# Optimization experiments

Hardware: AMD Instinct MI355X
Metric: run time of the kernel (lower is better)

## Reference

```python
import jax, jax.numpy as jnp
import numpy as np

N = 10000      # nodes
IN_DIM = 512   # input feature dim
HID = 512      # GCN hidden dim
OUT = 256      # embedding dim
E = 320000     # edges (avg degree 32)


def _normalize(x, eps=1e-12):
    # F.normalize: x / max(||x||_2, eps), row-wise
    n = jnp.sqrt(jnp.sum(x * x, axis=-1, keepdims=True))
    return x / jnp.maximum(n, eps)


def _gcn_conv(x, W, b, src, dst, n):
    # DGL GraphConv with norm='both': D_out^{-1/2} -> sum-aggregate -> D_in^{-1/2}, then bias
    ones = jnp.ones(src.shape[0], x.dtype)
    deg_out = jax.ops.segment_sum(ones, src, num_segments=n)
    deg_in = jax.ops.segment_sum(ones, dst, num_segments=n)
    ns = jnp.where(deg_out > 0, deg_out ** -0.5, 0.0)
    nd = jnp.where(deg_in > 0, deg_in ** -0.5, 0.0)
    h = x @ W                                  # weight first (math-equivalent)
    msg = h[src] * ns[src, None]               # gather + src-normalize
    agg = jax.ops.segment_sum(msg, dst, num_segments=n)  # scatter-sum to dst
    return agg * nd[:, None] + b


def _gcn(x, params, src, dst, n):
    W0, b0, W1, b1 = params
    h = jax.nn.relu(_gcn_conv(x, W0, b0, src, dst, n))
    return _gcn_conv(h, W1, b1, src, dst, n)


def _scores(v, u, Wp, bp, src, dst, n, tau):
    # pos_score: edge sim = <normalize(u)[src], normalize(proj(v))[dst]> / tau, scatter-mean to dst
    q = _normalize(v @ Wp + bp)
    un = _normalize(u)
    sim = jnp.sum(un[src] * q[dst], axis=1) / tau          # [E]
    cnt = jax.ops.segment_sum(jnp.ones_like(sim), dst, num_segments=n)
    denom = jnp.maximum(cnt, 1.0)                          # DGL mean gives 0 for deg-0 nodes
    pos = jax.ops.segment_sum(sim, dst, num_segments=n) / denom
    # neg_score: per-node total similarity (intra + inter), then per-edge log, scatter-mean
    z = _normalize(v)
    stu = _normalize(u)
    neg_sim = jnp.exp(z @ z.T / tau).sum(1) + jnp.exp(z @ stu.T / tau).sum(1)  # [N]
    m = jnp.log(neg_sim[dst] + jnp.exp(sim))               # udf_u_add_log_e
    neg = jax.ops.segment_sum(m, dst, num_segments=n) / denom
    return pos, neg


def setup_inputs() -> dict:
    key = jax.random.key(0)
    ks = jax.random.split(key, 16)
    feat = jax.random.normal(ks[0], (N, IN_DIM), jnp.float32)
    src_g = jax.random.randint(ks[1], (E,), 0, N)
    dst_g = jax.random.randint(ks[2], (E,), 0, N)
    src_s = jax.random.randint(ks[3], (E,), 0, N)
    dst_s = jax.random.randint(ks[4], (E,), 0, N)

    def lin(k, i, o, s=0.05):
        return jax.random.normal(k, (i, o), jnp.float32) * s

    inp = dict(
        feat=feat, src_g=src_g, dst_g=dst_g, src_s=src_s, dst_s=dst_s,
        tau1=jnp.ones((), jnp.float32), tau2=jnp.ones((), jnp.float32),
        # encoder1 (GCN, 2 layers) online + target (deepcopy -> independent params)
        W1a=lin(ks[5], IN_DIM, HID), b1a=jnp.zeros((HID,), jnp.float32),
        W1b=lin(ks[6], HID, OUT), b1b=jnp.zeros((OUT,), jnp.float32),
        W1a_t=lin(ks[7], IN_DIM, HID), b1a_t=jnp.zeros((HID,), jnp.float32),
        W1b_t=lin(ks[8], HID, OUT), b1b_t=jnp.zeros((OUT,), jnp.float32),
        # encoder2 (Linear) online + target
        W2=lin(ks[9], IN_DIM, OUT), b2=jnp.zeros((OUT,), jnp.float32),
        W2_t=lin(ks[10], IN_DIM, OUT), b2_t=jnp.zeros((OUT,), jnp.float32),
        # projector: Predictor(out, out, num_layers=1) -> single Linear
        Wp=lin(ks[11], OUT, OUT), bp=jnp.zeros((OUT,), jnp.float32),
    )
    return inp


def reference(feat, src_g, dst_g, src_s, dst_s, tau1, tau2,
              W1a, b1a, W1b, b1b, W1a_t, b1a_t, W1b_t, b1b_t,
              W2, b2, W2_t, b2_t, Wp, bp):
    n = feat.shape[0]
    # branch 1: GCN encoder
    v1 = _gcn(feat, (W1a, b1a, W1b, b1b), src_g, dst_g, n)
    u1 = _gcn(feat, (W1a_t, b1a_t, W1b_t, b1b_t), src_g, dst_g, n)
    pos1, neg1 = _scores(v1, u1, Wp, bp, src_s, dst_s, n, tau1)
    loss1 = jnp.mean(-pos1 + neg1)
    # branch 2: linear encoder
    v2 = feat @ W2 + b2
    u2 = feat @ W2_t + b2_t
    pos2, neg2 = _scores(v2, u2, Wp, bp, src_s, dst_s, n, tau2)
    loss2 = jnp.mean(-pos2 + neg2)
    return (v1, u1, v2, u2, loss1 + loss2)
```

## Files before the change

### kernel.cpp

```cpp
#include <hip/hip_runtime.h>

typedef __bf16 bf16x8 __attribute__((ext_vector_type(8)));
typedef float f32x4 __attribute__((ext_vector_type(4)));
typedef unsigned short u16x8 __attribute__((ext_vector_type(8)));

#define GLOAD16(gp, lp) __builtin_amdgcn_global_load_lds( \
    (const __attribute__((address_space(1))) void*)(gp), \
    (__attribute__((address_space(3))) void*)(lp), 16, 0, 0)

__device__ __forceinline__ unsigned short f2bf(float f) {
  union { float f; unsigned u; } c; c.f = f;
  unsigned u = c.u;
  u = (u + 0x7fffu + ((u >> 16) & 1u)) >> 16;
  return (unsigned short)u;
}
__device__ __forceinline__ float b2f(unsigned short u) {
  union { unsigned u; float f; } c; c.u = ((unsigned)u) << 16; return c.f;
}

__global__ void k_count(const int* __restrict__ src_g, const int* __restrict__ dst_g,
                        const int* __restrict__ dst_s,
                        int* deg_og, int* deg_ig, int* cnt_s, int E)
{
  int e = blockIdx.x * blockDim.x + threadIdx.x;
  if (e >= E) return;
  atomicAdd(&deg_og[src_g[e]], 1);
  atomicAdd(&deg_ig[dst_g[e]], 1);
  atomicAdd(&cnt_s[dst_s[e]], 1);
}

__global__ void k_norms(const int* __restrict__ deg_og, const int* __restrict__ deg_ig,
                        float* __restrict__ ns, float* __restrict__ nd, int N)
{
  int i = blockIdx.x * blockDim.x + threadIdx.x;
  if (i >= N) return;
  int a = deg_og[i]; ns[i] = a > 0 ? rsqrtf((float)a) : 0.f;
  int b = deg_ig[i]; nd[i] = b > 0 ? rsqrtf((float)b) : 0.f;
}

__global__ __launch_bounds__(1024) void k_scan(const int* __restrict__ deg, int* __restrict__ offs, int N)
{
  __shared__ int lds[1024];
  __shared__ int carry_s;
  const int t = threadIdx.x;
  if (t == 0) { carry_s = 0; offs[0] = 0; }
  __syncthreads();
  for (int base = 0; base < N; base += 1024) {
    const int i = base + t;
    int v = (i < N) ? deg[i] : 0;
    lds[t] = v;
    __syncthreads();
    for (int o = 1; o < 1024; o <<= 1) {
      int tmp = (t >= o) ? lds[t - o] : 0;
      __syncthreads();
      lds[t] += tmp;
      __syncthreads();
    }
    const int carry = carry_s;
    if (i < N) offs[i + 1] = lds[t] + carry;
    __syncthreads();
    if (t == 1023) carry_s = carry + lds[1023];
    __syncthreads();
  }
}

__global__ void k_fill(const int* __restrict__ src_g, const int* __restrict__ dst_g,
                       const int* __restrict__ offs, int* cursor, int* __restrict__ csr_src, int E)
{
  int e = blockIdx.x * blockDim.x + threadIdx.x;
  if (e >= E) return;
  int d = dst_g[e];
  int p = atomicAdd(&cursor[d], 1);
  csr_src[offs[d] + p] = src_g[e];
}

struct PrepArgs {
  const float *feat, *W1a, *W1at, *W1b, *W1bt, *W2, *W2t, *Wp;
  const float *b1a, *b1at, *b1b, *b1bt, *b2, *b2t;
  unsigned short *featb, *wcatL1, *wcat2, *wcatLin, *wtp;
  float *bcatL1, *bcatGcn, *bcatLin;
  int NF;
};
__global__ void k_prep(PrepArgs p)
{
  int i = blockIdx.x * blockDim.x + threadIdx.x;
  if (i < p.NF) { p.featb[i] = f2bf(p.feat[i]); return; }
  i -= p.NF;
  if (i < 1024 * 512) {
    int n = i >> 9, k = i & 511;
    p.wcatL1[i] = f2bf(n < 512 ? p.W1a[k * 512 + n] : p.W1at[k * 512 + n - 512]);
    return;
  }
  i -= 1024 * 512;
  if (i < 512 * 512) {
    int n = i >> 9, k = i & 511;
    p.wcat2[i] = f2bf(n < 256 ? p.W1b[k * 256 + n] : p.W1bt[k * 256 + n - 256]);
    return;
  }
  i -= 512 * 512;
  if (i < 512 * 512) {
    int n = i >> 9, k = i & 511;
    p.wcatLin[i] = f2bf(n < 256 ? p.W2[k * 256 + n] : p.W2t[k * 256 + n - 256]);
    return;
  }
  i -= 512 * 512;
  if (i < 256 * 256) {
    int n = i >> 8, k = i & 255;
    p.wtp[i] = f2bf(p.Wp[k * 256 + n]);
    return;
  }
  i -= 256 * 256;
  if (i < 1024) { p.bcatL1[i] = i < 512 ? p.b1a[i] : p.b1at[i - 512]; return; }
  i -= 1024;
  if (i < 512) { p.bcatGcn[i] = i < 256 ? p.b1b[i] : p.b1bt[i - 256]; return; }
  i -= 512;
  if (i < 512) { p.bcatLin[i] = i < 256 ? p.b2[i] : p.b2t[i - 256]; return; }
}

__global__ __launch_bounds__(256) void k_mgemm(
    const unsigned short* __restrict__ A, int lda,
    const unsigned short* __restrict__ Wt,
    const float* __restrict__ bias, float* __restrict__ outf, unsigned short* __restrict__ outb,
    int M, int K, int Nc, int relu, int asel, int splitM)
{
  __shared__ char smem[24576];
  char* As = smem;
  char* Bs = smem + 16384;
  const int tid = threadIdx.x;
  const int lane = tid & 63, w = tid >> 6;
  const int wr = w >> 1, wc = w & 1;
  const int bm = blockIdx.x * 128, bn = blockIdx.y * 64;
  const int aoff = (asel > 0 && bn >= asel) ? K : 0;
  const int srow = lane >> 3;
  const int scol = ((lane & 7) ^ srow) << 3;
  const int xr = (lane & 7) << 4;

  f32x4 acc[4][2];
  #pragma unroll
  for (int mi = 0; mi < 4; ++mi)
    #pragma unroll
    for (int nj = 0; nj < 2; ++nj)
      acc[mi][nj] = (f32x4){0.f, 0.f, 0.f, 0.f};

  for (int k0 = 0; k0 < K; k0 += 64) {
    #pragma unroll
    for (int i = 0; i < 4; ++i) {
      int row = w * 32 + i * 8 + srow;
      int rg = bm + row; rg = rg < M ? rg : M - 1;
      GLOAD16(A + (size_t)rg * lda + aoff + k0 + scol, As + (w * 4096 + i * 1024));
    }
    #pragma unroll
    for (int i = 0; i < 2; ++i) {
      int nrow = w * 16 + i * 8 + srow;
      GLOAD16(Wt + (size_t)(bn + nrow) * K + k0 + scol, Bs + (w * 2048 + i * 1024));
    }
    __syncthreads();
    #pragma unroll
    for (int ks = 0; ks < 2; ++ks) {
      const int kb = ks * 64 + ((lane >> 4) << 4);
      bf16x8 af[4], bfr[2];
      #pragma unroll
      for (int mi = 0; mi < 4; ++mi) {
        int row_l = wr * 64 + mi * 16 + (lane & 15);
        af[mi] = *(const bf16x8*)(As + row_l * 128 + (kb ^ xr));
      }
      #pragma unroll
      for (int nj = 0; nj < 2; ++nj) {
        int n_l = wc * 32 + nj * 16 + (lane & 15);
        bfr[nj] = *(const bf16x8*)(Bs + n_l * 128 + (kb ^ xr));
      }
      __builtin_amdgcn_s_setprio(1);
      #pragma unroll
      for (int mi = 0; mi < 4; ++mi)
        #pragma unroll
        for (int nj = 0; nj < 2; ++nj)
          acc[mi][nj] = __builtin_amdgcn_mfma_f32_16x16x32_bf16(af[mi], bfr[nj], acc[mi][nj], 0, 0, 0);
      __builtin_amdgcn_s_setprio(0);
    }
    __syncthreads();
  }

  #pragma unroll
  for (int mi = 0; mi < 4; ++mi) {
    #pragma unroll
    for (int j = 0; j < 4; ++j) {
      int r = bm + wr * 64 + mi * 16 + ((lane >> 4) << 2) + j;
      if (r >= M) continue;
      #pragma unroll
      for (int nj = 0; nj < 2; ++nj) {
        int c = bn + wc * 32 + nj * 16 + (lane & 15);
        float v = acc[mi][nj][j];
        if (bias) v += bias[c];
        if (relu) v = fmaxf(v, 0.f);
        if (splitM > 0) {
          int rr = r + (c >= 256 ? splitM : 0);
          if (outf) outf[(size_t)rr * 256 + (c & 255)] = v;
          if (outb && c < 256) outb[(size_t)r * 256 + c] = f2bf(v);
        } else {
          if (outf) outf[(size_t)r * Nc + c] = v;
          if (outb) outb[(size_t)r * Nc + c] = f2bf(v);
        }
      }
    }
  }
}

__global__ __launch_bounds__(256) void k_agg(const unsigned short* __restrict__ h,
    const int* __restrict__ offs, const int* __restrict__ csr,
    const float* __restrict__ ns, const float* __restrict__ nd, const float* __restrict__ bias,
    float* __restrict__ outf, unsigned short* __restrict__ outb, int relu, int splitM)
{
  const int node = blockIdx.x * 4 + (threadIdx.x >> 6);
  const int lane = threadIdx.x & 63;
  const int j = lane * 8;
  const int s0 = offs[node], s1 = offs[node + 1];
  float a[8] = {};
  for (int k = s0; k < s1; ++k) {
    const int s = csr[k];
    const float w = ns[s];
    const u16x8 hv = *(const u16x8*)(h + (size_t)s * 512 + j);
    #pragma unroll
    for (int q = 0; q < 8; ++q) a[q] += b2f(hv[q]) * w;
  }
  const float ndv = nd[node];
  float o[8];
  #pragma unroll
  for (int q = 0; q < 8; ++q) {
    o[q] = a[q] * ndv;
    if (bias) o[q] += bias[j + q];
    if (relu) o[q] = fmaxf(o[q], 0.f);
  }
  if (splitM > 0) {
    const int rr = node + (j >= 256 ? splitM : 0);
    const int cc = j & 255;
    if (outf) {
      *(float4*)(outf + (size_t)rr * 256 + cc)     = (float4){o[0], o[1], o[2], o[3]};
      *(float4*)(outf + (size_t)rr * 256 + cc + 4) = (float4){o[4], o[5], o[6], o[7]};
    }
    if (outb && j < 256) {
      u16x8 ub;
      #pragma unroll
      for (int q = 0; q < 8; ++q) ub[q] = f2bf(o[q]);
      *(u16x8*)(outb + (size_t)node * 256 + j) = ub;
    }
  } else {
    if (outf) {
      *(float4*)(outf + (size_t)node * 512 + j)     = (float4){o[0], o[1], o[2], o[3]};
      *(float4*)(outf + (size_t)node * 512 + j + 4) = (float4){o[4], o[5], o[6], o[7]};
    }
    if (outb) {
      u16x8 ub;
      #pragma unroll
      for (int q = 0; q < 8; ++q) ub[q] = f2bf(o[q]);
      *(u16x8*)(outb + (size_t)node * 512 + j) = ub;
    }
  }
}

__global__ __launch_bounds__(256) void k_normrows3(
    const float* __restrict__ X0, unsigned short* __restrict__ O0,
    const float* __restrict__ X1, unsigned short* __restrict__ O1,
    const float* __restrict__ X2, unsigned short* __restrict__ O2, int Nrows)
{
  const float* X = blockIdx.y == 0 ? X0 : (blockIdx.y == 1 ? X1 : X2);
  unsigned short* O = blockIdx.y == 0 ? O0 : (blockIdx.y == 1 ? O1 : O2);
  const int wid = threadIdx.x >> 6, lane = threadIdx.x & 63;
  const int row = blockIdx.x * 4 + wid;
  if (row >= Nrows) return;
  const float4 v = ((const float4*)(X + (size_t)row * 256))[lane];
  float ss = v.x * v.x + v.y * v.y + v.z * v.z + v.w * v.w;
  #pragma unroll
  for (int m = 1; m < 64; m <<= 1) ss += __shfl_xor(ss, m);
  const float inv = 1.f / fmaxf(sqrtf(ss), 1e-12f);
  ushort4 u;
  u.x = f2bf(v.x * inv); u.y = f2bf(v.y * inv);
  u.z = f2bf(v.z * inv); u.w = f2bf(v.w * inv);
  ((ushort4*)(O + (size_t)row * 256))[lane] = u;
}

__global__ __launch_bounds__(256) void k_edge(
    const unsigned short* __restrict__ zun1, const unsigned short* __restrict__ zun2,
    const unsigned short* __restrict__ qb,
    const int* __restrict__ src, const int* __restrict__ dst,
    const float* __restrict__ tau1p, const float* __restrict__ tau2p,
    const float* __restrict__ negs1, const float* __restrict__ negs2,
    float* __restrict__ pos1, float* __restrict__ neg1,
    float* __restrict__ pos2, float* __restrict__ neg2, int N, int E)
{
  const int e = blockIdx.x * 8 + (threadIdx.x >> 5);
  if (e >= E) return;
  const int z = blockIdx.y;
  const unsigned short* un = (z ? zun2 : zun1) + (size_t)N * 256;
  const unsigned short* q = qb + (size_t)z * N * 256;
  const float* negsim = z ? negs2 : negs1;
  float* pos = z ? pos2 : pos1;
  float* neg = z ? neg2 : neg1;
  const int l = threadIdx.x & 31;
  const int s = src[e], d = dst[e];
  const u16x8 a = *(const u16x8*)(un + (size_t)s * 256 + l * 8);
  const u16x8 b = *(const u16x8*)(q + (size_t)d * 256 + l * 8);
  float dot = 0.f;
  #pragma unroll
  for (int qq = 0; qq < 8; ++qq) dot += b2f(a[qq]) * b2f(b[qq]);
  #pragma unroll
  for (int m = 1; m < 32; m <<= 1) dot += __shfl_xor(dot, m);
  if (l == 0) {
    const float sv = dot / (z ? tau2p[0] : tau1p[0]);
    atomicAdd(&pos[d], sv);
    const float mlog = logf(negsim[d] + __expf(sv));
    atomicAdd(&neg[d], mlog);
  }
}

#define NEG_JSPLIT 16
#define NEG_TILES 4
__global__ __launch_bounds__(256) void k_negsim(
    const unsigned short* __restrict__ zun1, const unsigned short* __restrict__ zun2,
    const float* __restrict__ tau1p, const float* __restrict__ tau2p,
    float* __restrict__ negs1, float* __restrict__ negs2, int N)
{
  __shared__ char smem[32768];
  const int tid = threadIdx.x;
  const int lane = tid & 63, wid = tid >> 6;
  const int z = blockIdx.z;
  const unsigned short* zun = z ? zun2 : zun1;
  float* negsim = z ? negs2 : negs1;
  const float k_exp = 1.0f / (z ? tau2p[0] : tau1p[0]);
  const int ntiles = N >> 4;
  int itv[NEG_TILES]; bool vv[NEG_TILES];
  #pragma unroll
  for (int t = 0; t < NEG_TILES; ++t) {
    int it = blockIdx.x * (4 * NEG_TILES) + wid * NEG_TILES + t;
    vv[t] = it < ntiles;
    itv[t] = vv[t] ? it : (ntiles - 1);
  }

  bf16x8 afrag[NEG_TILES][8];
  #pragma unroll
  for (int t = 0; t < NEG_TILES; ++t) {
    const unsigned short* r = zun + (size_t)((itv[t] << 4) + (lane & 15)) * 256 + ((lane >> 4) << 3);
    #pragma unroll
    for (int ks = 0; ks < 8; ++ks)
      afrag[t][ks] = *(const bf16x8*)(r + ks * 32);
  }

  const int total = 2 * N;
  const int chunk = ((total + NEG_JSPLIT * 32 - 1) / (NEG_JSPLIT * 32)) * 32;
  const int jbeg = blockIdx.y * chunk;
  const int jend = min(total, jbeg + chunk);
  if (jbeg >= jend) return;

  float psum[NEG_TILES][4];
  #pragma unroll
  for (int t = 0; t < NEG_TILES; ++t)
    #pragma unroll
    for (int j = 0; j < 4; ++j) psum[t][j] = 0.f;

  auto stage = [&](int buf, int j0) {
    #pragma unroll
    for (int i = 0; i < 4; ++i) {
      int idx = tid + 256 * i;
      int r = idx >> 5, c = idx & 31;
      int g = j0 + r; g = g < total ? g : total - 1;
      int cp = c ^ (r & 7);
      GLOAD16(zun + (size_t)g * 256 + cp * 8, smem + buf * 16384 + r * 512 + c * 16);
    }
  };

  const int rxor = (lane & 7) << 4;
  const int kcol = (lane >> 4) << 4;
  int cur = 0;
  stage(0, jbeg);
  __syncthreads();
  for (int j0 = jbeg; j0 < jend; j0 += 32) {
    if (j0 + 32 < jend) stage(cur ^ 1, j0 + 32);
    const int rows = min(32, jend - j0);
    const int nsub = rows >> 4;
    const char* base = smem + cur * 16384;
    for (int sub = 0; sub < nsub; ++sub) {
      const char* bb = base + (sub * 16 + (lane & 15)) * 512;
      f32x4 acc[NEG_TILES];
      #pragma unroll
      for (int t = 0; t < NEG_TILES; ++t) acc[t] = (f32x4){0.f, 0.f, 0.f, 0.f};
      __builtin_amdgcn_s_setprio(1);
      #pragma unroll
      for (int ks = 0; ks < 8; ++ks) {
        bf16x8 bfrag = *(const bf16x8*)(bb + ((kcol + ks * 64) ^ rxor));
        #pragma unroll
        for (int t = 0; t < NEG_TILES; ++t)
          acc[t] = __builtin_amdgcn_mfma_f32_16x16x32_bf16(afrag[t][ks], bfrag, acc[t], 0, 0, 0);
      }
      __builtin_amdgcn_s_setprio(0);
      #pragma unroll
      for (int t = 0; t < NEG_TILES; ++t)
        #pragma unroll
        for (int j = 0; j < 4; ++j)
          psum[t][j] += __expf(acc[t][j] * k_exp);
    }
    __syncthreads();
    cur ^= 1;
  }
  #pragma unroll
  for (int t = 0; t < NEG_TILES; ++t)
    #pragma unroll
    for (int j = 0; j < 4; ++j) {
      float x = psum[t][j];
      x += __shfl_xor(x, 1);
      x += __shfl_xor(x, 2);
      x += __shfl_xor(x, 4);
      x += __shfl_xor(x, 8);
      if (vv[t] && (lane & 15) == 0)
        atomicAdd(&negsim[(itv[t] << 4) + ((lane >> 4) << 2) + j], x);
    }
}

__global__ __launch_bounds__(1024) void k_loss(
    const float* __restrict__ pos1, const float* __restrict__ neg1,
    const float* __restrict__ pos2, const float* __restrict__ neg2,
    const int* __restrict__ cnt, int N, float* __restrict__ out)
{
  __shared__ float lds[1024];
  float s = 0.f;
  for (int i = threadIdx.x; i < N; i += 1024) {
    float denom = fmaxf((float)cnt[i], 1.f);
    s += ((-pos1[i] + neg1[i]) + (-pos2[i] + neg2[i])) / denom;
  }
  lds[threadIdx.x] = s;
  __syncthreads();
  for (int o = 512; o > 0; o >>= 1) {
    if (threadIdx.x < o) lds[threadIdx.x] += lds[threadIdx.x + o];
    __syncthreads();
  }
  if (threadIdx.x == 0) out[0] = lds[0] / (float)N;
}

extern "C" void kernel_launch(void* const* d_in, const int* in_sizes, int n_in,
                              void* d_out, int out_size, void* d_ws, size_t ws_size,
                              hipStream_t stream)
{
  const float* feat  = (const float*)d_in[0];
  const int* src_g   = (const int*)d_in[1];
  const int* dst_g   = (const int*)d_in[2];
  const int* src_s   = (const int*)d_in[3];
  const int* dst_s   = (const int*)d_in[4];
  const float* tau1  = (const float*)d_in[5];
  const float* tau2  = (const float*)d_in[6];
  const float* W1a   = (const float*)d_in[7];
  const float* b1a   = (const float*)d_in[8];
  const float* W1b   = (const float*)d_in[9];
  const float* b1b   = (const float*)d_in[10];
  const float* W1a_t = (const float*)d_in[11];
  const float* b1a_t = (const float*)d_in[12];
  const float* W1b_t = (const float*)d_in[13];
  const float* b1b_t = (const float*)d_in[14];
  const float* W2    = (const float*)d_in[15];
  const float* b2    = (const float*)d_in[16];
  const float* W2_t  = (const float*)d_in[17];
  const float* b2_t  = (const float*)d_in[18];
  const float* Wp    = (const float*)d_in[19];
  const float* bp    = (const float*)d_in[20];

  const int N = in_sizes[0] / 512;
  const int E = in_sizes[1];

  float* out  = (float*)d_out;
  float* v1u1 = out;
  float* v2u2 = out + (size_t)2 * N * 256;
  float* loss = out + (size_t)4 * N * 256;

  char* ws = (char*)d_ws;
  size_t off = 0;
  auto alloc = [&](size_t bytes) -> char* {
    char* p = ws + off;
    off += (bytes + 255) & ~(size_t)255;
    return p;
  };
  int* zbase   = (int*)alloc((size_t)10 * N * 4);
  int* deg_og  = zbase;
  int* deg_ig  = zbase + N;
  int* cnt_s   = zbase + 2 * N;
  int* cursor  = zbase + 3 * N;
  float* pos1  = (float*)(zbase + 4 * N);
  float* neg1  = (float*)(zbase + 5 * N);
  float* pos2  = (float*)(zbase + 6 * N);
  float* neg2  = (float*)(zbase + 7 * N);
  float* negs1 = (float*)(zbase + 8 * N);
  float* negs2 = (float*)(zbase + 9 * N);
  int* offs    = (int*)alloc((size_t)(N + 1) * 4);
  int* csr_src = (int*)alloc((size_t)E * 4);
  float* ns    = (float*)alloc((size_t)N * 4);
  float* nd    = (float*)alloc((size_t)N * 4);
  unsigned short* featb   = (unsigned short*)alloc((size_t)N * 512 * 2);
  unsigned short* wcatL1  = (unsigned short*)alloc((size_t)1024 * 512 * 2);
  unsigned short* wcat2   = (unsigned short*)alloc((size_t)512 * 512 * 2);
  unsigned short* wcatLin = (unsigned short*)alloc((size_t)512 * 512 * 2);
  unsigned short* wtp     = (unsigned short*)alloc((size_t)256 * 256 * 2);
  float* bcatL1  = (float*)alloc(1024 * 4);
  float* bcatGcn = (float*)alloc(512 * 4);
  float* bcatLin = (float*)alloc(512 * 4);
  char* BUF_H = alloc((size_t)N * 2048);
  char* BUF_A = alloc((size_t)N * 1024);
  char* BUF_B = alloc((size_t)N * 1024);
  char* BUF_C = alloc((size_t)N * 1024);
  char* BUF_E = alloc((size_t)N * 1024);
  if (off > ws_size) return;

  unsigned short* Xaggb = (unsigned short*)BUF_A;
  unsigned short* hcat  = (unsigned short*)BUF_H;
  unsigned short* g2cat = (unsigned short*)BUF_A;
  unsigned short* v1b   = (unsigned short*)BUF_E;
  float*          q_raw = (float*)BUF_H;
  unsigned short* qb    = (unsigned short*)BUF_A;
  unsigned short* zun1  = (unsigned short*)BUF_B;
  unsigned short* zun2  = (unsigned short*)BUF_C;

  const int eb = (E + 255) / 256;
  const int gmx = (N + 127) / 128;
  const int gqx = (2 * N + 127) / 128;
  const int ntiles = N / 16;
  const int ngroups = (ntiles + 4 * NEG_TILES - 1) / (4 * NEG_TILES);
  const dim3 neggrid(ngroups, NEG_JSPLIT, 2);
  const dim3 edgegrid((E + 7) / 8, 2);
  const dim3 nrmgrid((2 * N + 3) / 4, 3);

  hipMemsetAsync(zbase, 0, (size_t)10 * N * 4, stream);
  k_count<<<eb, 256, 0, stream>>>(src_g, dst_g, dst_s, deg_og, deg_ig, cnt_s, E);
  k_norms<<<(N + 255) / 256, 256, 0, stream>>>(deg_og, deg_ig, ns, nd, N);
  k_scan<<<1, 1024, 0, stream>>>(deg_ig, offs, N);
  k_fill<<<eb, 256, 0, stream>>>(src_g, dst_g, offs, cursor, csr_src, E);

  PrepArgs pa;
  pa.feat = feat; pa.W1a = W1a; pa.W1at = W1a_t; pa.W1b = W1b; pa.W1bt = W1b_t;
  pa.W2 = W2; pa.W2t = W2_t; pa.Wp = Wp;
  pa.b1a = b1a; pa.b1at = b1a_t; pa.b1b = b1b; pa.b1bt = b1b_t; pa.b2 = b2; pa.b2t = b2_t;
  pa.featb = featb; pa.wcatL1 = wcatL1; pa.wcat2 = wcat2; pa.wcatLin = wcatLin; pa.wtp = wtp;
  pa.bcatL1 = bcatL1; pa.bcatGcn = bcatGcn; pa.bcatLin = bcatLin;
  pa.NF = N * 512;
  const int ptotal = pa.NF + 1024 * 512 + 512 * 512 + 512 * 512 + 256 * 256 + 1024 + 512 + 512;
  k_prep<<<(ptotal + 255) / 256, 256, 0, stream>>>(pa);

  k_agg<<<N / 4, 256, 0, stream>>>(featb, offs, csr_src, ns, nd, nullptr, nullptr, Xaggb, 0, 0);
  k_mgemm<<<dim3(gmx, 16), 256, 0, stream>>>(Xaggb, 512, wcatL1, bcatL1, nullptr, hcat,
                                             N, 512, 1024, 1, 0, 0);
  k_mgemm<<<dim3(gmx, 8), 256, 0, stream>>>(hcat, 1024, wcat2, nullptr, nullptr, g2cat,
                                            N, 512, 512, 0, 256, 0);
  k_agg<<<N / 4, 256, 0, stream>>>(g2cat, offs, csr_src, ns, nd, bcatGcn, v1u1, v1b, 0, N);
  k_mgemm<<<dim3(gmx, 8), 256, 0, stream>>>(featb, 512, wcatLin, bcatLin, v2u2,
                                            (unsigned short*)BUF_E + (size_t)N * 256,
                                            N, 512, 512, 0, 0, N);
  k_mgemm<<<dim3(gqx, 4), 256, 0, stream>>>((unsigned short*)BUF_E, 256, wtp, bp, q_raw, nullptr,
                                            2 * N, 256, 256, 0, 0, 0);

  k_normrows3<<<nrmgrid, 256, 0, stream>>>(v1u1, zun1, v2u2, zun2, q_raw, qb, 2 * N);

  k_negsim<<<neggrid, 256, 0, stream>>>(zun1, zun2, tau1, tau2, negs1, negs2, N);
  k_edge<<<edgegrid, 256, 0, stream>>>(zun1, zun2, qb, src_s, dst_s, tau1, tau2,
                                       negs1, negs2, pos1, neg1, pos2, neg2, N, E);
  k_loss<<<1, 1024, 0, stream>>>(pos1, neg1, pos2, neg2, cnt_s, N, loss);
}
```

Before: 645.7 us.

## Exploit symmetry of z·zᵀ in negsim and double the staged tile to 64 rows

The negative-similarity kernel now splits the column range into the student half (full) and the self-similarity half. The self half is restricted to upper-triangular tiles, with off-diagonal tiles contributing exp sums to both row and column nodes via extra atomics, which roughly halves the z·zᵀ MFMA and exp work. The shared staging buffer grows to 64 rows per stage (64KB LDS) and exp is computed with exp2f and a prescaled constant. The symmetric credit adds per-subtile column atomics, causes load imbalance between blocks over the triangular ranges, and the larger LDS footprint may lower occupancy.

After: 670.6 us. 3.9% more time.

```diff
diff --git a/kernel.cpp b/kernel.cpp
--- a/kernel.cpp
+++ b/kernel.cpp
@@ -319,14 +319,15 @@
     const float* __restrict__ tau1p, const float* __restrict__ tau2p,
     float* __restrict__ negs1, float* __restrict__ negs2, int N)
 {
-  __shared__ char smem[32768];
+  __shared__ char smem[65536];
   const int tid = threadIdx.x;
   const int lane = tid & 63, wid = tid >> 6;
   const int z = blockIdx.z;
   const unsigned short* zun = z ? zun2 : zun1;
   float* negsim = z ? negs2 : negs1;
-  const float k_exp = 1.0f / (z ? tau2p[0] : tau1p[0]);
+  const float KE = 1.4426950408889634f / (z ? tau2p[0] : tau1p[0]);
   const int ntiles = N >> 4;
+  const int i0_w = blockIdx.x * 256 + wid * 64;
   int itv[NEG_TILES]; bool vv[NEG_TILES];
   #pragma unroll
   for (int t = 0; t < NEG_TILES; ++t) {
@@ -344,62 +345,90 @@
       afrag[t][ks] = *(const bf16x8*)(r + ks * 32);
   }
 
-  const int total = 2 * N;
-  const int chunk = ((total + NEG_JSPLIT * 32 - 1) / (NEG_JSPLIT * 32)) * 32;
-  const int jbeg = blockIdx.y * chunk;
-  const int jend = min(total, jbeg + chunk);
-  if (jbeg >= jend) return;
-
   float psum[NEG_TILES][4];
   #pragma unroll
   for (int t = 0; t < NEG_TILES; ++t)
     #pragma unroll
     for (int j = 0; j < 4; ++j) psum[t][j] = 0.f;
-
-  auto stage = [&](int buf, int j0) {
-    #pragma unroll
-    for (int i = 0; i < 4; ++i) {
-      int idx = tid + 256 * i;
-      int r = idx >> 5, c = idx & 31;
-      int g = j0 + r; g = g < total ? g : total - 1;
-      int cp = c ^ (r & 7);
-      GLOAD16(zun + (size_t)g * 256 + cp * 8, smem + buf * 16384 + r * 512 + c * 16);
-    }
-  };
 
   const int rxor = (lane & 7) << 4;
   const int kcol = (lane >> 4) << 4;
-  int cur = 0;
-  stage(0, jbeg);
-  __syncthreads();
-  for (int j0 = jbeg; j0 < jend; j0 += 32) {
-    if (j0 + 32 < jend) stage(cur ^ 1, j0 + 32);
-    const int rows = min(32, jend - j0);
-    const int nsub = rows >> 4;
-    const char* base = smem + cur * 16384;
-    for (int sub = 0; sub < nsub; ++sub) {
-      const char* bb = base + (sub * 16 + (lane & 15)) * 512;
-      f32x4 acc[NEG_TILES];
-      #pragma unroll
-      for (int t = 0; t < NEG_TILES; ++t) acc[t] = (f32x4){0.f, 0.f, 0.f, 0.f};
-      __builtin_amdgcn_s_setprio(1);
-      #pragma unroll
-      for (int ks = 0; ks < 8; ++ks) {
-        bf16x8 bfrag = *(const bf16x8*)(bb + ((kcol + ks * 64) ^ rxor));
+
+  const int ch = ((N + NEG_JSPLIT * 64 - 1) / (NEG_JSPLIT * 64)) * 64;
+  const int hb = blockIdx.y * ch, he = min(N, hb + ch);
+  const int blo = blockIdx.x * 256;
+  const int grange = N - blo;
+  const int cg = ((grange + NEG_JSPLIT * 64 - 1) / (NEG_JSPLIT * 64)) * 64;
+  const int gb = blo + blockIdx.y * cg, ge = min(N, gb + cg);
+
+  auto run = [&](const unsigned short* src, int jb, int je, bool gmode) {
+    if (jb >= je) return;
+    auto stage = [&](int buf, int j0) {
+      #pragma unroll
+      for (int i = 0; i < 8; ++i) {
+        int idx = tid + 256 * i;
+        int r = idx >> 5, c = idx & 31;
+        int g = j0 + r; g = g < N ? g : N - 1;
+        int cp = c ^ (r & 7);
+        GLOAD16(src + (size_t)g * 256 + cp * 8, smem + buf * 32768 + r * 512 + c * 16);
+      }
+    };
+    int cur = 0;
+    stage(0, jb);
+    __syncthreads();
+    for (int j0 = jb; j0 < je; j0 += 64) {
+      if (j0 + 64 < je) stage(cur ^ 1, j0 + 64);
+      const int rows = min(64, je - j0);
+      const int nsub = rows >> 4;
+      const char* base = smem + cur * 32768;
+      for (int sub = 0; sub < nsub; ++sub) {
+        const int jrow = j0 + sub * 16;
+        if (gmode && jrow < i0_w) continue;
+        const char* bb = base + (sub * 16 + (lane & 15)) * 512;
+        f32x4 acc[NEG_TILES];
         #pragma unroll
-        for (int t = 0; t < NEG_TILES; ++t)
-          acc[t] = __builtin_amdgcn_mfma_f32_16x16x32_bf16(afrag[t][ks], bfrag, acc[t], 0, 0, 0);
+        for (int t = 0; t < NEG_TILES; ++t) acc[t] = (f32x4){0.f, 0.f, 0.f, 0.f};
+        __builtin_amdgcn_s_setprio(1);
+        #pragma unroll
+        for (int ks = 0; ks < 8; ++ks) {
+          bf16x8 bfrag = *(const bf16x8*)(bb + ((kcol + ks * 64) ^ rxor));
+          #pragma unroll
+          for (int t = 0; t < NEG_TILES; ++t)
+            acc[t] = __builtin_amdgcn_mfma_f32_16x16x32_bf16(afrag[t][ks], bfrag, acc[t], 0, 0, 0);
+        }
+        __builtin_amdgcn_s_setprio(0);
+        if (gmode && jrow >= i0_w + 64) {
+          float part = 0.f;
+          #pragma unroll
+          for (int t = 0; t < NEG_TILES; ++t) {
+            float s = 0.f;
+            #pragma unroll
+            for (int j = 0; j < 4; ++j) {
+              const float ev = exp2f(acc[t][j] * KE);
+              psum[t][j] += ev;
+              s += ev;
+            }
+            if (vv[t]) part += s;
+          }
+          part += __shfl_xor(part, 16);
+          part += __shfl_xor(part, 32);
+          if (lane < 16) atomicAdd(&negsim[jrow + lane], part);
+        } else {
+          #pragma unroll
+          for (int t = 0; t < NEG_TILES; ++t)
+            #pragma unroll
+            for (int j = 0; j < 4; ++j)
+              psum[t][j] += exp2f(acc[t][j] * KE);
+        }
       }
-      __builtin_amdgcn_s_setprio(0);
-      #pragma unroll
-      for (int t = 0; t < NEG_TILES; ++t)
-        #pragma unroll
-        for (int j = 0; j < 4; ++j)
-          psum[t][j] += __expf(acc[t][j] * k_exp);
-    }
-    __syncthreads();
-    cur ^= 1;
-  }
+      __syncthreads();
+      cur ^= 1;
+    }
+  };
+
+  run(zun + (size_t)N * 256, hb, he, false);
+  run(zun, gb, ge, true);
+
   #pragma unroll
   for (int t = 0; t < NEG_TILES; ++t)
     #pragma unroll
```

## Build CSR for score graph and compute edge scores per destination node

Applied to the files above, without the earlier changes.

Builds a second CSR (grouped by destination) for the score-graph edges by extending the scan and fill kernels to handle two graphs. The edge-score kernel then runs one wavefront per destination node, loads the node's q row once, and accumulates pos and neg in registers. This removes per-edge float atomics and the repeated q gathers. The cost is an extra scan and fill pass, plus possible load imbalance across nodes with different degrees.

Measured after the change: 625.8 us. 3.1% less time.

```diff
diff --git a/kernel.cpp b/kernel.cpp
--- a/kernel.cpp
+++ b/kernel.cpp
@@ -38,8 +38,11 @@
   int b = deg_ig[i]; nd[i] = b > 0 ? rsqrtf((float)b) : 0.f;
 }
 
-__global__ __launch_bounds__(1024) void k_scan(const int* __restrict__ deg, int* __restrict__ offs, int N)
-{
+__global__ __launch_bounds__(1024) void k_scan(const int* __restrict__ deg0, int* __restrict__ offs0,
+                                               const int* __restrict__ deg1, int* __restrict__ offs1, int N)
+{
+  const int* deg = blockIdx.x ? deg1 : deg0;
+  int* offs = blockIdx.x ? offs1 : offs0;
   __shared__ int lds[1024];
   __shared__ int carry_s;
   const int t = threadIdx.x;
@@ -64,14 +67,22 @@
   }
 }
 
-__global__ void k_fill(const int* __restrict__ src_g, const int* __restrict__ dst_g,
-                       const int* __restrict__ offs, int* cursor, int* __restrict__ csr_src, int E)
+__global__ void k_fill(const int* __restrict__ srcA, const int* __restrict__ dstA,
+                       const int* __restrict__ offsA, int* curA, int* __restrict__ outA,
+                       const int* __restrict__ srcB, const int* __restrict__ dstB,
+                       const int* __restrict__ offsB, int* curB, int* __restrict__ outB, int E)
 {
   int e = blockIdx.x * blockDim.x + threadIdx.x;
   if (e >= E) return;
-  int d = dst_g[e];
-  int p = atomicAdd(&cursor[d], 1);
-  csr_src[offs[d] + p] = src_g[e];
+  if (blockIdx.y == 0) {
+    int d = dstA[e];
+    int p = atomicAdd(&curA[d], 1);
+    outA[offsA[d] + p] = srcA[e];
+  } else {
+    int d = dstB[e];
+    int p = atomicAdd(&curB[d], 1);
+    outB[offsB[d] + p] = srcB[e];
+  }
 }
 
 struct PrepArgs {
@@ -281,35 +292,46 @@
 __global__ __launch_bounds__(256) void k_edge(
     const unsigned short* __restrict__ zun1, const unsigned short* __restrict__ zun2,
     const unsigned short* __restrict__ qb,
-    const int* __restrict__ src, const int* __restrict__ dst,
+    const int* __restrict__ offs_s, const int* __restrict__ csr_es,
     const float* __restrict__ tau1p, const float* __restrict__ tau2p,
     const float* __restrict__ negs1, const float* __restrict__ negs2,
     float* __restrict__ pos1, float* __restrict__ neg1,
-    float* __restrict__ pos2, float* __restrict__ neg2, int N, int E)
-{
-  const int e = blockIdx.x * 8 + (threadIdx.x >> 5);
-  if (e >= E) return;
+    float* __restrict__ pos2, float* __restrict__ neg2, int N)
+{
+  const int node = blockIdx.x * 4 + (threadIdx.x >> 6);
+  if (node >= N) return;
   const int z = blockIdx.y;
   const unsigned short* un = (z ? zun2 : zun1) + (size_t)N * 256;
   const unsigned short* q = qb + (size_t)z * N * 256;
-  const float* negsim = z ? negs2 : negs1;
+  const float inv_tau = 1.f / (z ? tau2p[0] : tau1p[0]);
+  const float nsd = (z ? negs2 : negs1)[node];
   float* pos = z ? pos2 : pos1;
   float* neg = z ? neg2 : neg1;
-  const int l = threadIdx.x & 31;
-  const int s = src[e], d = dst[e];
-  const u16x8 a = *(const u16x8*)(un + (size_t)s * 256 + l * 8);
-  const u16x8 b = *(const u16x8*)(q + (size_t)d * 256 + l * 8);
-  float dot = 0.f;
-  #pragma unroll
-  for (int qq = 0; qq < 8; ++qq) dot += b2f(a[qq]) * b2f(b[qq]);
-  #pragma unroll
-  for (int m = 1; m < 32; m <<= 1) dot += __shfl_xor(dot, m);
-  if (l == 0) {
-    const float sv = dot / (z ? tau2p[0] : tau1p[0]);
-    atomicAdd(&pos[d], sv);
-    const float mlog = logf(negsim[d] + __expf(sv));
-    atomicAdd(&neg[d], mlog);
-  }
+  const int lane = threadIdx.x & 63;
+  const int l = lane & 31, h = lane >> 5;
+  const u16x8 qv = *(const u16x8*)(q + (size_t)node * 256 + l * 8);
+  float qf[8];
+  #pragma unroll
+  for (int i = 0; i < 8; ++i) qf[i] = b2f(qv[i]);
+  const int s0 = offs_s[node], s1 = offs_s[node + 1];
+  float pacc = 0.f, nacc = 0.f;
+  for (int k = s0 + h; k < s1; k += 2) {
+    const int s = csr_es[k];
+    const u16x8 av = *(const u16x8*)(un + (size_t)s * 256 + l * 8);
+    float dot = 0.f;
+    #pragma unroll
+    for (int i = 0; i < 8; ++i) dot += b2f(av[i]) * qf[i];
+    #pragma unroll
+    for (int m = 1; m < 32; m <<= 1) dot += __shfl_xor(dot, m);
+    if (l == 0) {
+      const float sv = dot * inv_tau;
+      pacc += sv;
+      nacc += logf(nsd + __expf(sv));
+    }
+  }
+  pacc += __shfl_xor(pacc, 32);
+  nacc += __shfl_xor(nacc, 32);
+  if (lane == 0) { pos[node] = pacc; neg[node] = nacc; }
 }
 
 #define NEG_JSPLIT 16
@@ -475,19 +497,22 @@
     off += (bytes + 255) & ~(size_t)255;
     return p;
   };
-  int* zbase   = (int*)alloc((size_t)10 * N * 4);
-  int* deg_og  = zbase;
-  int* deg_ig  = zbase + N;
-  int* cnt_s   = zbase + 2 * N;
-  int* cursor  = zbase + 3 * N;
-  float* pos1  = (float*)(zbase + 4 * N);
-  float* neg1  = (float*)(zbase + 5 * N);
-  float* pos2  = (float*)(zbase + 6 * N);
-  float* neg2  = (float*)(zbase + 7 * N);
-  float* negs1 = (float*)(zbase + 8 * N);
-  float* negs2 = (float*)(zbase + 9 * N);
+  int* zbase    = (int*)alloc((size_t)11 * N * 4);
+  int* deg_og   = zbase;
+  int* deg_ig   = zbase + N;
+  int* cnt_s    = zbase + 2 * N;
+  int* cursor   = zbase + 3 * N;
+  int* cursor_s = zbase + 4 * N;
+  float* pos1   = (float*)(zbase + 5 * N);
+  float* neg1   = (float*)(zbase + 6 * N);
+  float* pos2   = (float*)(zbase + 7 * N);
+  float* neg2   = (float*)(zbase + 8 * N);
+  float* negs1  = (float*)(zbase + 9 * N);
+  float* negs2  = (float*)(zbase + 10 * N);
   int* offs    = (int*)alloc((size_t)(N + 1) * 4);
+  int* offs_s  = (int*)alloc((size_t)(N + 1) * 4);
   int* csr_src = (int*)alloc((size_t)E * 4);
+  int* csr_es  = (int*)alloc((size_t)E * 4);
   float* ns    = (float*)alloc((size_t)N * 4);
   float* nd    = (float*)alloc((size_t)N * 4);
   unsigned short* featb   = (unsigned short*)alloc((size_t)N * 512 * 2);
@@ -520,14 +545,15 @@
   const int ntiles = N / 16;
   const int ngroups = (ntiles + 4 * NEG_TILES - 1) / (4 * NEG_TILES);
   const dim3 neggrid(ngroups, NEG_JSPLIT, 2);
-  const dim3 edgegrid((E + 7) / 8, 2);
+  const dim3 edgegrid((N + 3) / 4, 2);
   const dim3 nrmgrid((2 * N + 3) / 4, 3);
 
-  hipMemsetAsync(zbase, 0, (size_t)10 * N * 4, stream);
+  hipMemsetAsync(zbase, 0, (size_t)11 * N * 4, stream);
   k_count<<<eb, 256, 0, stream>>>(src_g, dst_g, dst_s, deg_og, deg_ig, cnt_s, E);
   k_norms<<<(N + 255) / 256, 256, 0, stream>>>(deg_og, deg_ig, ns, nd, N);
-  k_scan<<<1, 1024, 0, stream>>>(deg_ig, offs, N);
-  k_fill<<<eb, 256, 0, stream>>>(src_g, dst_g, offs, cursor, csr_src, E);
+  k_scan<<<2, 1024, 0, stream>>>(deg_ig, offs, cnt_s, offs_s, N);
+  k_fill<<<dim3(eb, 2), 256, 0, stream>>>(src_g, dst_g, offs, cursor, csr_src,
+                                          src_s, dst_s, offs_s, cursor_s, csr_es, E);
 
   PrepArgs pa;
   pa.feat = feat; pa.W1a = W1a; pa.W1at = W1a_t; pa.W1b = W1b; pa.W1bt = W1b_t;
@@ -554,7 +580,7 @@
   k_normrows3<<<nrmgrid, 256, 0, stream>>>(v1u1, zun1, v2u2, zun2, q_raw, qb, 2 * N);
 
   k_negsim<<<neggrid, 256, 0, stream>>>(zun1, zun2, tau1, tau2, negs1, negs2, N);
-  k_edge<<<edgegrid, 256, 0, stream>>>(zun1, zun2, qb, src_s, dst_s, tau1, tau2,
-                                       negs1, negs2, pos1, neg1, pos2, neg2, N, E);
+  k_edge<<<edgegrid, 256, 0, stream>>>(zun1, zun2, qb, offs_s, csr_es, tau1, tau2,
+                                       negs1, negs2, pos1, neg1, pos2, neg2, N);
   k_loss<<<1, 1024, 0, stream>>>(pos1, neg1, pos2, neg2, cnt_s, N, loss);
 }
```
